# Optimization experiments

Measured on AMD Instinct MI355X. Metric: run time of the kernel, lower is better.

The kernel has to match this reference:

```python
import jax, jax.numpy as jnp
import numpy as np
import math

D_MODEL = 1024
NUM_HEADS = 16
D_K = D_MODEL // NUM_HEADS
MAX_LEN = 2048
BATCH = 2
SEQ = 2048


def setup_inputs() -> dict:
    key = jax.random.key(0)
    ks = jax.random.split(key, 12)
    w_scale = 0.02  # realistic init scale for linear weights
    inp = {
        "q": jax.random.normal(ks[0], (BATCH, SEQ, D_MODEL), jnp.float32),
        "k": jax.random.normal(ks[1], (BATCH, SEQ, D_MODEL), jnp.float32),
        "v": jax.random.normal(ks[2], (BATCH, SEQ, D_MODEL), jnp.float32),
        # learned params
        "rel_emb": jax.random.normal(ks[3], (2 * MAX_LEN, D_K), jnp.float32),
        "wq": jax.random.normal(ks[4], (D_MODEL, D_MODEL), jnp.float32) * w_scale,
        "bq": jnp.zeros((D_MODEL,), jnp.float32),
        "wk": jax.random.normal(ks[5], (D_MODEL, D_MODEL), jnp.float32) * w_scale,
        "bk": jnp.zeros((D_MODEL,), jnp.float32),
        "wv": jax.random.normal(ks[6], (D_MODEL, D_MODEL), jnp.float32) * w_scale,
        "bv": jnp.zeros((D_MODEL,), jnp.float32),
        "wo": jax.random.normal(ks[7], (D_MODEL, D_MODEL), jnp.float32) * w_scale,
        "bo": jnp.zeros((D_MODEL,), jnp.float32),
    }
    return inp


def reference(q, k, v, rel_emb, wq, bq, wk, bk, wv, bv, wo, bo):
    B, L, D = q.shape
    H, dk = NUM_HEADS, D // NUM_HEADS

    def split_heads(x):  # [B, L, D] -> [B, H, L, dk]
        return x.reshape(B, L, H, dk).transpose(0, 2, 1, 3)

    qh = split_heads(q @ wq.T + bq)
    kh = split_heads(k @ wk.T + bk)
    vh = split_heads(v @ wv.T + bv)

    # relative positions: rel_pos[i, j] = (j - i) + MAX_LEN, in [0, 2*MAX_LEN)
    r = jnp.arange(L)
    rel_pos = r[None, :] - r[:, None] + MAX_LEN  # [L, L] int32

    content_score = jnp.einsum("bhid,bhjd->bhij", qh, kh)
    # pos_score[b,h,i,j] = q[b,h,i,:] . rel_emb[rel_pos[i,j], :]
    rel = rel_emb[rel_pos]  # [L, L, dk]
    pos_score = jnp.einsum("bhid,ijd->bhij", qh, rel)

    scores = (content_score + pos_score) / math.sqrt(dk)
    attn = jax.nn.softmax(scores, axis=-1)
    out = jnp.einsum("bhij,bhjd->bhid", attn, vh)  # [B, H, L, dk]
    out = out.transpose(0, 2, 1, 3).reshape(B, L, D)
    return out @ wo.T + bo
```

## Files before the change

kernel.cpp:

```cpp
#include <hip/hip_runtime.h>
#include <hip/hip_fp16.h>


typedef _Float16 f16;
typedef _Float16 f16x4 __attribute__((ext_vector_type(4)));
typedef _Float16 f16x8 __attribute__((ext_vector_type(8)));
typedef float    f32x4 __attribute__((ext_vector_type(4)));

#define NBATCH 2
#define NHEADS 16
#define DKDIM  64
#define SEQL   2048
#define DMODEL 1024
#define NTOK   4096
#define MAXLEN 2048

__device__ __forceinline__ void gload16(const f16* g, f16* l) {
    __builtin_amdgcn_global_load_lds(
        (const __attribute__((address_space(1))) void*)g,
        (__attribute__((address_space(3))) void*)l, 16, 0, 0);
}

__global__ void cvt_f32_f16(const float* __restrict__ src, f16* __restrict__ dst, int n4) {
    int i = blockIdx.x * blockDim.x + threadIdx.x;
    if (i < n4) {
        float4 v = ((const float4*)src)[i];
        f16x4 h = { (f16)v.x, (f16)v.y, (f16)v.z, (f16)v.w };
        ((f16x4*)dst)[i] = h;
    }
}

__global__ __launch_bounds__(256, 2) void qkv_proj(
    const float* __restrict__ qg, const float* __restrict__ kg, const float* __restrict__ vg,
    const float* __restrict__ wq, const float* __restrict__ wk, const float* __restrict__ wv,
    const float* __restrict__ bq, const float* __restrict__ bk, const float* __restrict__ bv,
    f16* __restrict__ qh, f16* __restrict__ kh, f16* __restrict__ vt)
{
    const int which = blockIdx.z;
    const float* X    = which == 0 ? qg : (which == 1 ? kg : vg);
    const float* W    = which == 0 ? wq : (which == 1 ? wk : wv);
    const float* bias = which == 0 ? bq : (which == 1 ? bk : bv);

    __shared__ f16 As[128][72];
    __shared__ f16 Bs[128][72];

    const int tid = threadIdx.x;
    const int lane = tid & 63;
    const int w = tid >> 6;
    const int wr = w >> 1, wc = w & 1;
    const int row0 = blockIdx.y * 128;
    const int col0 = blockIdx.x * 128;

    f32x4 acc[4][4] = {};
    float4 ra[8], rw[8];

    #pragma unroll
    for (int rep = 0; rep < 8; ++rep) {
        int idx = rep * 256 + tid;
        int r = idx >> 4, seg = idx & 15;
        ra[rep] = *(const float4*)&X[(size_t)(row0 + r) * DMODEL + seg * 4];
        rw[rep] = *(const float4*)&W[(size_t)(col0 + r) * DMODEL + seg * 4];
    }

    for (int kk = 0; kk < DMODEL; kk += 64) {
        #pragma unroll
        for (int rep = 0; rep < 8; ++rep) {
            int idx = rep * 256 + tid;
            int r = idx >> 4, seg = idx & 15;
            f16x4 ha = { (f16)ra[rep].x, (f16)ra[rep].y, (f16)ra[rep].z, (f16)ra[rep].w };
            *(f16x4*)&As[r][seg * 4] = ha;
            f16x4 hb = { (f16)rw[rep].x, (f16)rw[rep].y, (f16)rw[rep].z, (f16)rw[rep].w };
            *(f16x4*)&Bs[r][seg * 4] = hb;
        }
        __syncthreads();
        if (kk + 64 < DMODEL) {
            #pragma unroll
            for (int rep = 0; rep < 8; ++rep) {
                int idx = rep * 256 + tid;
                int r = idx >> 4, seg = idx & 15;
                ra[rep] = *(const float4*)&X[(size_t)(row0 + r) * DMODEL + kk + 64 + seg * 4];
                rw[rep] = *(const float4*)&W[(size_t)(col0 + r) * DMODEL + kk + 64 + seg * 4];
            }
        }
        f16x8 a[4][2], b[4][2];
        #pragma unroll
        for (int mi = 0; mi < 4; ++mi)
            #pragma unroll
            for (int ks = 0; ks < 2; ++ks)
                a[mi][ks] = *(const f16x8*)&As[wr * 64 + mi * 16 + (lane & 15)][ks * 32 + (lane >> 4) * 8];
        #pragma unroll
        for (int ni = 0; ni < 4; ++ni)
            #pragma unroll
            for (int ks = 0; ks < 2; ++ks)
                b[ni][ks] = *(const f16x8*)&Bs[wc * 64 + ni * 16 + (lane & 15)][ks * 32 + (lane >> 4) * 8];
        __builtin_amdgcn_s_setprio(1);
        #pragma unroll
        for (int mi = 0; mi < 4; ++mi)
            #pragma unroll
            for (int ni = 0; ni < 4; ++ni)
                #pragma unroll
                for (int ks = 0; ks < 2; ++ks)
                    acc[mi][ni] = __builtin_amdgcn_mfma_f32_16x16x32_f16(a[mi][ks], b[ni][ks], acc[mi][ni], 0, 0, 0);
        __builtin_amdgcn_s_setprio(0);
        __syncthreads();
    }

    #pragma unroll
    for (int mi = 0; mi < 4; ++mi) {
        #pragma unroll
        for (int ni = 0; ni < 4; ++ni) {
            int col = col0 + wc * 64 + ni * 16 + (lane & 15);
            int h = col >> 6, d = col & 63;
            float bc = bias[col];
            int rowb = row0 + wr * 64 + mi * 16 + (lane >> 4) * 4;
            int b_ = rowb >> 11, l0 = rowb & 2047;
            if (which == 2) {
                f16x4 pk = { (f16)(acc[mi][ni][0] + bc), (f16)(acc[mi][ni][1] + bc),
                             (f16)(acc[mi][ni][2] + bc), (f16)(acc[mi][ni][3] + bc) };
                *(f16x4*)&vt[((size_t)((b_ * 16 + h) * 64 + d)) * 2048 + l0] = pk;
            } else {
                f16* dst = (which == 0) ? qh : kh;
                #pragma unroll
                for (int r = 0; r < 4; ++r)
                    dst[((size_t)((b_ * 16 + h) * 2048 + l0 + r)) * 64 + d] = (f16)(acc[mi][ni][r] + bc);
            }
        }
    }
}

__global__ __launch_bounds__(256, 2) void flash_attn(
    const f16* __restrict__ qh, const f16* __restrict__ kh, const f16* __restrict__ vt,
    const f16* __restrict__ rel, f16* __restrict__ att)
{
    const int tid = threadIdx.x, lane = tid & 63, w = tid >> 6;
    const int i_l = lane & 15, hi = lane >> 4;
    const int bh = blockIdx.y;
    const int b = bh >> 4, h = bh & 15;
    const int i0 = blockIdx.x * 64;

    __shared__ f16 Stage[2][16384];
    __shared__ f16 Qb[4][16][88];

    const size_t base_kq = (size_t)bh * SEQL * DKDIM;
    const int pb0 = MAXLEN - i0 - 63;
    const int t0 = 48 - w * 16;

    const int lr = lane >> 3;
    const int lc = lane & 7;
    const int sc = (lc ^ lr) << 3;

    const f16* qrow = &qh[base_kq + (size_t)(i0 + w * 16 + i_l) * 64];
    f16x8 aq[2];
    aq[0] = *(const f16x8*)&qrow[hi * 8];
    aq[1] = *(const f16x8*)&qrow[32 + hi * 8];

    {
        f16* sb = &Stage[0][0];
        #pragma unroll
        for (int c = 0; c < 2; ++c) {
            int row = w * 16 + c * 8;
            gload16(&kh[base_kq + (size_t)(row + lr) * 64 + sc], &sb[row * 64]);
            gload16(&vt[base_kq + (size_t)(row + lr) * 2048 + 0 + sc], &sb[4096 + row * 64]);
        }
        #pragma unroll
        for (int c = 0; c < 4; ++c) {
            int rrow = w * 32 + c * 8;
            int p = pb0 + rrow + lr; if (p > 4095) p = 4095;
            gload16(&rel[(size_t)p * 64 + sc], &sb[8192 + rrow * 64]);
        }
    }

    float mrun = -1e30f, lrun = 0.f;
    f32x4 oacc[4] = {};
    int cur = 0;

    const int sw0 = (hi ^ (i_l & 7)) << 3;
    const int sw1 = sw0 ^ 32;

    for (int j0 = 0; j0 < SEQL; j0 += 64) {
        __syncthreads();

        if (j0 + 64 < SEQL) {
            f16* sb = &Stage[cur ^ 1][0];
            const int jn = j0 + 64;
            #pragma unroll
            for (int c = 0; c < 2; ++c) {
                int row = w * 16 + c * 8;
                gload16(&kh[base_kq + (size_t)(jn + row + lr) * 64 + sc], &sb[row * 64]);
                gload16(&vt[base_kq + (size_t)(row + lr) * 2048 + jn + sc], &sb[4096 + row * 64]);
            }
            #pragma unroll
            for (int c = 0; c < 4; ++c) {
                int rrow = w * 32 + c * 8;
                int p = pb0 + jn + rrow + lr; if (p > 4095) p = 4095;
                gload16(&rel[(size_t)p * 64 + sc], &sb[8192 + rrow * 64]);
            }
        }

        const f16* sb = &Stage[cur][0];

        f32x4 sacc[4] = {};
        __builtin_amdgcn_s_setprio(1);
        #pragma unroll
        for (int jf = 0; jf < 4; ++jf) {
            f16x8 ak0 = *(const f16x8*)&sb[(jf * 16 + i_l) * 64 + sw0];
            f16x8 ak1 = *(const f16x8*)&sb[(jf * 16 + i_l) * 64 + sw1];
            sacc[jf] = __builtin_amdgcn_mfma_f32_16x16x32_f16(ak0, aq[0], sacc[jf], 0, 0, 0);
            sacc[jf] = __builtin_amdgcn_mfma_f32_16x16x32_f16(ak1, aq[1], sacc[jf], 0, 0, 0);
        }
        f32x4 qracc[5] = {};
        #pragma unroll
        for (int pf = 0; pf < 5; ++pf) {
            int rrow = 8192 + (t0 + pf * 16 + i_l) * 64;
            f16x8 ar0 = *(const f16x8*)&sb[rrow + sw0];
            f16x8 ar1 = *(const f16x8*)&sb[rrow + sw1];
            qracc[pf] = __builtin_amdgcn_mfma_f32_16x16x32_f16(ar0, aq[0], qracc[pf], 0, 0, 0);
            qracc[pf] = __builtin_amdgcn_mfma_f32_16x16x32_f16(ar1, aq[1], qracc[pf], 0, 0, 0);
        }
        __builtin_amdgcn_s_setprio(0);

        #pragma unroll
        for (int pf = 0; pf < 5; ++pf) {
            f16x4 pk = { (f16)qracc[pf][0], (f16)qracc[pf][1], (f16)qracc[pf][2], (f16)qracc[pf][3] };
            *(f16x4*)&Qb[w][i_l][pf * 16 + 4 * hi] = pk;
        }

        float p_[4][4];
        #pragma unroll
        for (int nf = 0; nf < 4; ++nf)
            #pragma unroll
            for (int r = 0; r < 4; ++r) {
                int t = nf * 16 + 4 * hi + r - i_l + 15;
                p_[nf][r] = (sacc[nf][r] + (float)Qb[w][i_l][t]) * 0.125f;
            }

        float mx = fmaxf(fmaxf(fmaxf(p_[0][0], p_[0][1]), fmaxf(p_[0][2], p_[0][3])),
                         fmaxf(fmaxf(p_[1][0], p_[1][1]), fmaxf(p_[1][2], p_[1][3])));
        mx = fmaxf(mx, fmaxf(fmaxf(fmaxf(p_[2][0], p_[2][1]), fmaxf(p_[2][2], p_[2][3])),
                             fmaxf(fmaxf(p_[3][0], p_[3][1]), fmaxf(p_[3][2], p_[3][3]))));
        mx = fmaxf(mx, __shfl_xor(mx, 16, 64));
        mx = fmaxf(mx, __shfl_xor(mx, 32, 64));
        if (!__all(mx - mrun <= 8.f)) {
            float mnew = fmaxf(mrun, mx);
            float scv = __expf(mrun - mnew);
            float scb[4];
            #pragma unroll
            for (int r = 0; r < 4; ++r)
                scb[r] = __shfl(scv, (lane & 48) | (4 * hi + r), 64);
            #pragma unroll
            for (int df = 0; df < 4; ++df)
                #pragma unroll
                for (int r = 0; r < 4; ++r) oacc[df][r] *= scb[r];
            lrun *= scv;
            mrun = mnew;
        }
        float sm = 0.f;
        #pragma unroll
        for (int nf = 0; nf < 4; ++nf) {
            #pragma unroll
            for (int r = 0; r < 4; ++r) { p_[nf][r] = __expf(p_[nf][r] - mrun); }
            sm += (p_[nf][0] + p_[nf][1]) + (p_[nf][2] + p_[nf][3]);
        }
        sm += __shfl_xor(sm, 16, 64);
        sm += __shfl_xor(sm, 32, 64);
        lrun += sm;

        #pragma unroll
        for (int nf = 0; nf < 4; ++nf) {
            f16x4 pk = { (f16)p_[nf][0], (f16)p_[nf][1], (f16)p_[nf][2], (f16)p_[nf][3] };
            *(f16x4*)&Qb[w][i_l][nf * 16 + 4 * hi] = pk;
        }
        f16x8 pa[2];
        pa[0] = *(const f16x8*)&Qb[w][i_l][hi * 8];
        pa[1] = *(const f16x8*)&Qb[w][i_l][32 + hi * 8];
        __builtin_amdgcn_s_setprio(1);
        #pragma unroll
        for (int df = 0; df < 4; ++df) {
            f16x8 bv0 = *(const f16x8*)&sb[4096 + (df * 16 + i_l) * 64 + sw0];
            f16x8 bv1 = *(const f16x8*)&sb[4096 + (df * 16 + i_l) * 64 + sw1];
            oacc[df] = __builtin_amdgcn_mfma_f32_16x16x32_f16(pa[0], bv0, oacc[df], 0, 0, 0);
            oacc[df] = __builtin_amdgcn_mfma_f32_16x16x32_f16(pa[1], bv1, oacc[df], 0, 0, 0);
        }
        __builtin_amdgcn_s_setprio(0);
        cur ^= 1;
    }

    float lb[4];
    #pragma unroll
    for (int r = 0; r < 4; ++r)
        lb[r] = __shfl(lrun, (lane & 48) | (4 * hi + r), 64);
    #pragma unroll
    for (int df = 0; df < 4; ++df) {
        int d = df * 16 + i_l;
        #pragma unroll
        for (int r = 0; r < 4; ++r) {
            int i = i0 + w * 16 + 4 * hi + r;
            float val = oacc[df][r] / lb[r];
            att[((size_t)(b * 2048 + i)) * DMODEL + h * 64 + d] = (f16)val;
        }
    }
}

__global__ __launch_bounds__(256, 2) void out_proj(
    const f16* __restrict__ att, const float* __restrict__ wo, const float* __restrict__ bo,
    float* __restrict__ out)
{
    __shared__ f16 As[128][72];
    __shared__ f16 Bs[128][72];
    const int tid = threadIdx.x, lane = tid & 63, w = tid >> 6;
    const int wr = w >> 1, wc = w & 1;
    const int row0 = blockIdx.y * 128, col0 = blockIdx.x * 128;

    f32x4 acc[4][4] = {};
    int4 pa_[4];
    float4 pw[8];

    #pragma unroll
    for (int rep = 0; rep < 4; ++rep) {
        int idx = rep * 256 + tid;
        int r = idx >> 3, seg = idx & 7;
        pa_[rep] = *(const int4*)&att[(size_t)(row0 + r) * DMODEL + seg * 8];
    }
    #pragma unroll
    for (int rep = 0; rep < 8; ++rep) {
        int idx = rep * 256 + tid;
        int r = idx >> 4, seg = idx & 15;
        pw[rep] = *(const float4*)&wo[(size_t)(col0 + r) * DMODEL + seg * 4];
    }

    for (int kk = 0; kk < DMODEL; kk += 64) {
        #pragma unroll
        for (int rep = 0; rep < 4; ++rep) {
            int idx = rep * 256 + tid;
            int r = idx >> 3, seg = idx & 7;
            *(int4*)&As[r][seg * 8] = pa_[rep];
        }
        #pragma unroll
        for (int rep = 0; rep < 8; ++rep) {
            int idx = rep * 256 + tid;
            int r = idx >> 4, seg = idx & 15;
            f16x4 hb = { (f16)pw[rep].x, (f16)pw[rep].y, (f16)pw[rep].z, (f16)pw[rep].w };
            *(f16x4*)&Bs[r][seg * 4] = hb;
        }
        __syncthreads();
        if (kk + 64 < DMODEL) {
            #pragma unroll
            for (int rep = 0; rep < 4; ++rep) {
                int idx = rep * 256 + tid;
                int r = idx >> 3, seg = idx & 7;
                pa_[rep] = *(const int4*)&att[(size_t)(row0 + r) * DMODEL + kk + 64 + seg * 8];
            }
            #pragma unroll
            for (int rep = 0; rep < 8; ++rep) {
                int idx = rep * 256 + tid;
                int r = idx >> 4, seg = idx & 15;
                pw[rep] = *(const float4*)&wo[(size_t)(col0 + r) * DMODEL + kk + 64 + seg * 4];
            }
        }
        f16x8 a[4][2], b[4][2];
        #pragma unroll
        for (int mi = 0; mi < 4; ++mi)
            #pragma unroll
            for (int ks = 0; ks < 2; ++ks)
                a[mi][ks] = *(const f16x8*)&As[wr * 64 + mi * 16 + (lane & 15)][ks * 32 + (lane >> 4) * 8];
        #pragma unroll
        for (int ni = 0; ni < 4; ++ni)
            #pragma unroll
            for (int ks = 0; ks < 2; ++ks)
                b[ni][ks] = *(const f16x8*)&Bs[wc * 64 + ni * 16 + (lane & 15)][ks * 32 + (lane >> 4) * 8];
        __builtin_amdgcn_s_setprio(1);
        #pragma unroll
        for (int mi = 0; mi < 4; ++mi)
            #pragma unroll
            for (int ni = 0; ni < 4; ++ni)
                #pragma unroll
                for (int ks = 0; ks < 2; ++ks)
                    acc[mi][ni] = __builtin_amdgcn_mfma_f32_16x16x32_f16(a[mi][ks], b[ni][ks], acc[mi][ni], 0, 0, 0);
        __builtin_amdgcn_s_setprio(0);
        __syncthreads();
    }

    #pragma unroll
    for (int mi = 0; mi < 4; ++mi)
        #pragma unroll
        for (int ni = 0; ni < 4; ++ni) {
            int col = col0 + wc * 64 + ni * 16 + (lane & 15);
            float bc = bo[col];
            #pragma unroll
            for (int r = 0; r < 4; ++r) {
                int row = row0 + wr * 64 + mi * 16 + (lane >> 4) * 4 + r;
                out[(size_t)row * DMODEL + col] = acc[mi][ni][r] + bc;
            }
        }
}

extern "C" void kernel_launch(void* const* d_in, const int* in_sizes, int n_in,
                              void* d_out, int out_size, void* d_ws, size_t ws_size,
                              hipStream_t stream) {
    const float* q   = (const float*)d_in[0];
    const float* k   = (const float*)d_in[1];
    const float* v   = (const float*)d_in[2];
    const float* rel = (const float*)d_in[3];
    const float* wq  = (const float*)d_in[4];
    const float* bq  = (const float*)d_in[5];
    const float* wk  = (const float*)d_in[6];
    const float* bk  = (const float*)d_in[7];
    const float* wv  = (const float*)d_in[8];
    const float* bv  = (const float*)d_in[9];
    const float* wo  = (const float*)d_in[10];
    const float* bo  = (const float*)d_in[11];
    float* out = (float*)d_out;

    f16* ws    = (f16*)d_ws;
    f16* rel16 = ws;
    f16* qh16  = rel16 + (size_t)2 * MAXLEN * DKDIM;
    f16* kh16  = qh16 + (size_t)NTOK * DMODEL;
    f16* vt16  = kh16 + (size_t)NTOK * DMODEL;
    f16* att16 = vt16 + (size_t)NTOK * DMODEL;

    cvt_f32_f16<<<dim3(256), 256, 0, stream>>>(rel, rel16, 2 * MAXLEN * DKDIM / 4);
    qkv_proj<<<dim3(8, 32, 3), 256, 0, stream>>>(q, k, v, wq, wk, wv, bq, bk, bv,
                                                 qh16, kh16, vt16);
    flash_attn<<<dim3(32, 32), 256, 0, stream>>>(qh16, kh16, vt16, rel16, att16);
    out_proj<<<dim3(8, 32), 256, 0, stream>>>(att16, wo, bo, out);
}
```

Baseline: 386.3 us.

## Pre-convert inputs and weights to fp16, use direct global-to-LDS loads in GEMMs

Adds a single conversion kernel that casts q/k/v, all four weight matrices and rel_emb to fp16 in the workspace. The projection GEMMs then stream fp16 tiles straight into LDS with global_load_lds, using an XOR-swizzled layout instead of padding, and raise occupancy to 3 blocks. They also use a swizzled block order for L2 locality. This removes per-tile fp32 loads and conversions, but it drops the register prefetch double-buffering and adds an extra full pass over the inputs. att16 now aliases the converted q buffer.

```diff
diff --git a/kernel.cpp b/kernel.cpp
--- a/kernel.cpp
+++ b/kernel.cpp
@@ -21,86 +21,88 @@
         (__attribute__((address_space(3))) void*)l, 16, 0, 0);
 }
 
-__global__ void cvt_f32_f16(const float* __restrict__ src, f16* __restrict__ dst, int n4) {
-    int i = blockIdx.x * blockDim.x + threadIdx.x;
-    if (i < n4) {
-        float4 v = ((const float4*)src)[i];
-        f16x4 h = { (f16)v.x, (f16)v.y, (f16)v.z, (f16)v.w };
+__global__ void cvt_all(
+    const float* __restrict__ q, const float* __restrict__ k, const float* __restrict__ v,
+    const float* __restrict__ wq, const float* __restrict__ wk, const float* __restrict__ wv,
+    const float* __restrict__ wo, const float* __restrict__ rel, f16* __restrict__ dst)
+{
+    const int SX = 1048576;
+    const int SW = 262144;
+    const int SR = 65536;
+    const int total = 3 * SX + 4 * SW + SR;
+    for (int i = blockIdx.x * blockDim.x + threadIdx.x; i < total; i += gridDim.x * blockDim.x) {
+        int j = i;
+        const float* s;
+        if (j < SX) s = q;
+        else if ((j -= SX) < SX) s = k;
+        else if ((j -= SX) < SX) s = v;
+        else if ((j -= SX) < SW) s = wq;
+        else if ((j -= SW) < SW) s = wk;
+        else if ((j -= SW) < SW) s = wv;
+        else if ((j -= SW) < SW) s = wo;
+        else { j -= SW; s = rel; }
+        float4 vv = ((const float4*)s)[j];
+        f16x4 h = { (f16)vv.x, (f16)vv.y, (f16)vv.z, (f16)vv.w };
         ((f16x4*)dst)[i] = h;
     }
 }
 
-__global__ __launch_bounds__(256, 2) void qkv_proj(
-    const float* __restrict__ qg, const float* __restrict__ kg, const float* __restrict__ vg,
-    const float* __restrict__ wq, const float* __restrict__ wk, const float* __restrict__ wv,
+__global__ __launch_bounds__(256, 3) void qkv_proj(
+    const f16* __restrict__ xq, const f16* __restrict__ xk, const f16* __restrict__ xv,
+    const f16* __restrict__ wq16, const f16* __restrict__ wk16, const f16* __restrict__ wv16,
     const float* __restrict__ bq, const float* __restrict__ bk, const float* __restrict__ bv,
     f16* __restrict__ qh, f16* __restrict__ kh, f16* __restrict__ vt)
 {
     const int which = blockIdx.z;
-    const float* X    = which == 0 ? qg : (which == 1 ? kg : vg);
-    const float* W    = which == 0 ? wq : (which == 1 ? wk : wv);
+    const f16* X      = which == 0 ? xq : (which == 1 ? xk : xv);
+    const f16* W      = which == 0 ? wq16 : (which == 1 ? wk16 : wv16);
     const float* bias = which == 0 ? bq : (which == 1 ? bk : bv);
 
-    __shared__ f16 As[128][72];
-    __shared__ f16 Bs[128][72];
-
-    const int tid = threadIdx.x;
-    const int lane = tid & 63;
-    const int w = tid >> 6;
+    __shared__ f16 As[128 * 64];
+    __shared__ f16 Bs[128 * 64];
+
+    const int tid = threadIdx.x, lane = tid & 63, w = tid >> 6;
+    const int i_l = lane & 15, hi = lane >> 4;
     const int wr = w >> 1, wc = w & 1;
-    const int row0 = blockIdx.y * 128;
-    const int col0 = blockIdx.x * 128;
+
+    const int nbid = blockIdx.y * 8 + blockIdx.x;
+    const int swz = (nbid & 7) * 32 + (nbid >> 3);
+    const int row0 = (swz >> 3) * 128;
+    const int col0 = (swz & 7) * 128;
+
+    const int lr = lane >> 3, lc = lane & 7;
+    const int sc = (lc ^ lr) << 3;
 
     f32x4 acc[4][4] = {};
-    float4 ra[8], rw[8];
-
-    #pragma unroll
-    for (int rep = 0; rep < 8; ++rep) {
-        int idx = rep * 256 + tid;
-        int r = idx >> 4, seg = idx & 15;
-        ra[rep] = *(const float4*)&X[(size_t)(row0 + r) * DMODEL + seg * 4];
-        rw[rep] = *(const float4*)&W[(size_t)(col0 + r) * DMODEL + seg * 4];
-    }
 
     for (int kk = 0; kk < DMODEL; kk += 64) {
         #pragma unroll
-        for (int rep = 0; rep < 8; ++rep) {
-            int idx = rep * 256 + tid;
-            int r = idx >> 4, seg = idx & 15;
-            f16x4 ha = { (f16)ra[rep].x, (f16)ra[rep].y, (f16)ra[rep].z, (f16)ra[rep].w };
-            *(f16x4*)&As[r][seg * 4] = ha;
-            f16x4 hb = { (f16)rw[rep].x, (f16)rw[rep].y, (f16)rw[rep].z, (f16)rw[rep].w };
-            *(f16x4*)&Bs[r][seg * 4] = hb;
+        for (int c = 0; c < 4; ++c) {
+            int row = w * 32 + c * 8;
+            gload16(&X[(size_t)(row0 + row + lr) * DMODEL + kk + sc], &As[row * 64]);
+            gload16(&W[(size_t)(col0 + row + lr) * DMODEL + kk + sc], &Bs[row * 64]);
         }
         __syncthreads();
-        if (kk + 64 < DMODEL) {
-            #pragma unroll
-            for (int rep = 0; rep < 8; ++rep) {
-                int idx = rep * 256 + tid;
-                int r = idx >> 4, seg = idx & 15;
-                ra[rep] = *(const float4*)&X[(size_t)(row0 + r) * DMODEL + kk + 64 + seg * 4];
-                rw[rep] = *(const float4*)&W[(size_t)(col0 + r) * DMODEL + kk + 64 + seg * 4];
-            }
-        }
-        f16x8 a[4][2], b[4][2];
-        #pragma unroll
-        for (int mi = 0; mi < 4; ++mi)
+
+        f16x8 bfr[4][2];
+        #pragma unroll
+        for (int ni = 0; ni < 4; ++ni)
             #pragma unroll
             for (int ks = 0; ks < 2; ++ks)
-                a[mi][ks] = *(const f16x8*)&As[wr * 64 + mi * 16 + (lane & 15)][ks * 32 + (lane >> 4) * 8];
-        #pragma unroll
-        for (int ni = 0; ni < 4; ++ni)
+                bfr[ni][ks] = *(const f16x8*)&Bs[(wc * 64 + ni * 16 + i_l) * 64 + (((ks * 4 + hi) ^ (i_l & 7)) << 3)];
+        __builtin_amdgcn_s_setprio(1);
+        #pragma unroll
+        for (int mi = 0; mi < 4; ++mi) {
+            f16x8 afr[2];
             #pragma unroll
             for (int ks = 0; ks < 2; ++ks)
-                b[ni][ks] = *(const f16x8*)&Bs[wc * 64 + ni * 16 + (lane & 15)][ks * 32 + (lane >> 4) * 8];
-        __builtin_amdgcn_s_setprio(1);
-        #pragma unroll
-        for (int mi = 0; mi < 4; ++mi)
+                afr[ks] = *(const f16x8*)&As[(wr * 64 + mi * 16 + i_l) * 64 + (((ks * 4 + hi) ^ (i_l & 7)) << 3)];
             #pragma unroll
             for (int ni = 0; ni < 4; ++ni)
                 #pragma unroll
                 for (int ks = 0; ks < 2; ++ks)
-                    acc[mi][ni] = __builtin_amdgcn_mfma_f32_16x16x32_f16(a[mi][ks], b[ni][ks], acc[mi][ni], 0, 0, 0);
+                    acc[mi][ni] = __builtin_amdgcn_mfma_f32_16x16x32_f16(afr[ks], bfr[ni][ks], acc[mi][ni], 0, 0, 0);
+        }
         __builtin_amdgcn_s_setprio(0);
         __syncthreads();
     }
@@ -109,10 +111,10 @@
     for (int mi = 0; mi < 4; ++mi) {
         #pragma unroll
         for (int ni = 0; ni < 4; ++ni) {
-            int col = col0 + wc * 64 + ni * 16 + (lane & 15);
+            int col = col0 + wc * 64 + ni * 16 + i_l;
             int h = col >> 6, d = col & 63;
             float bc = bias[col];
-            int rowb = row0 + wr * 64 + mi * 16 + (lane >> 4) * 4;
+            int rowb = row0 + wr * 64 + mi * 16 + hi * 4;
             int b_ = rowb >> 11, l0 = rowb & 2047;
             if (which == 2) {
                 f16x4 pk = { (f16)(acc[mi][ni][0] + bc), (f16)(acc[mi][ni][1] + bc),
@@ -301,81 +303,55 @@
     }
 }
 
-__global__ __launch_bounds__(256, 2) void out_proj(
-    const f16* __restrict__ att, const float* __restrict__ wo, const float* __restrict__ bo,
+__global__ __launch_bounds__(256, 3) void out_proj(
+    const f16* __restrict__ att, const f16* __restrict__ wo16, const float* __restrict__ bo,
     float* __restrict__ out)
 {
-    __shared__ f16 As[128][72];
-    __shared__ f16 Bs[128][72];
+    __shared__ f16 As[128 * 64];
+    __shared__ f16 Bs[128 * 64];
+
     const int tid = threadIdx.x, lane = tid & 63, w = tid >> 6;
+    const int i_l = lane & 15, hi = lane >> 4;
     const int wr = w >> 1, wc = w & 1;
-    const int row0 = blockIdx.y * 128, col0 = blockIdx.x * 128;
+
+    const int nbid = blockIdx.y * 8 + blockIdx.x;
+    const int swz = (nbid & 7) * 32 + (nbid >> 3);
+    const int row0 = (swz >> 3) * 128;
+    const int col0 = (swz & 7) * 128;
+
+    const int lr = lane >> 3, lc = lane & 7;
+    const int sc = (lc ^ lr) << 3;
 
     f32x4 acc[4][4] = {};
-    int4 pa_[4];
-    float4 pw[8];
-
-    #pragma unroll
-    for (int rep = 0; rep < 4; ++rep) {
-        int idx = rep * 256 + tid;
-        int r = idx >> 3, seg = idx & 7;
-        pa_[rep] = *(const int4*)&att[(size_t)(row0 + r) * DMODEL + seg * 8];
-    }
-    #pragma unroll
-    for (int rep = 0; rep < 8; ++rep) {
-        int idx = rep * 256 + tid;
-        int r = idx >> 4, seg = idx & 15;
-        pw[rep] = *(const float4*)&wo[(size_t)(col0 + r) * DMODEL + seg * 4];
-    }
 
     for (int kk = 0; kk < DMODEL; kk += 64) {
         #pragma unroll
-        for (int rep = 0; rep < 4; ++rep) {
-            int idx = rep * 256 + tid;
-            int r = idx >> 3, seg = idx & 7;
-            *(int4*)&As[r][seg * 8] = pa_[rep];
-        }
-        #pragma unroll
-        for (int rep = 0; rep < 8; ++rep) {
-            int idx = rep * 256 + tid;
-            int r = idx >> 4, seg = idx & 15;
-            f16x4 hb = { (f16)pw[rep].x, (f16)pw[rep].y, (f16)pw[rep].z, (f16)pw[rep].w };
-            *(f16x4*)&Bs[r][seg * 4] = hb;
+        for (int c = 0; c < 4; ++c) {
+            int row = w * 32 + c * 8;
+            gload16(&att[(size_t)(row0 + row + lr) * DMODEL + kk + sc], &As[row * 64]);
+            gload16(&wo16[(size_t)(col0 + row + lr) * DMODEL + kk + sc], &Bs[row * 64]);
         }
         __syncthreads();
-        if (kk + 64 < DMODEL) {
-            #pragma unroll
-            for (int rep = 0; rep < 4; ++rep) {
-                int idx = rep * 256 + tid;
-                int r = idx >> 3, seg = idx & 7;
-                pa_[rep] = *(const int4*)&att[(size_t)(row0 + r) * DMODEL + kk + 64 + seg * 8];
-            }
-            #pragma unroll
-            for (int rep = 0; rep < 8; ++rep) {
-                int idx = rep * 256 + tid;
-                int r = idx >> 4, seg = idx & 15;
-                pw[rep] = *(const float4*)&wo[(size_t)(col0 + r) * DMODEL + kk + 64 + seg * 4];
-            }
-        }
-        f16x8 a[4][2], b[4][2];
-        #pragma unroll
-        for (int mi = 0; mi < 4; ++mi)
+
+        f16x8 bfr[4][2];
+        #pragma unroll
+        for (int ni = 0; ni < 4; ++ni)
             #pragma unroll
             for (int ks = 0; ks < 2; ++ks)
-                a[mi][ks] = *(const f16x8*)&As[wr * 64 + mi * 16 + (lane & 15)][ks * 32 + (lane >> 4) * 8];
-        #pragma unroll
-        for (int ni = 0; ni < 4; ++ni)
+                bfr[ni][ks] = *(const f16x8*)&Bs[(wc * 64 + ni * 16 + i_l) * 64 + (((ks * 4 + hi) ^ (i_l & 7)) << 3)];
+        __builtin_amdgcn_s_setprio(1);
+        #pragma unroll
+        for (int mi = 0; mi < 4; ++mi) {
+            f16x8 afr[2];
             #pragma unroll
             for (int ks = 0; ks < 2; ++ks)
-                b[ni][ks] = *(const f16x8*)&Bs[wc * 64 + ni * 16 + (lane & 15)][ks * 32 + (lane >> 4) * 8];
-        __builtin_amdgcn_s_setprio(1);
-        #pragma unroll
-        for (int mi = 0; mi < 4; ++mi)
+                afr[ks] = *(const f16x8*)&As[(wr * 64 + mi * 16 + i_l) * 64 + (((ks * 4 + hi) ^ (i_l & 7)) << 3)];
             #pragma unroll
             for (int ni = 0; ni < 4; ++ni)
                 #pragma unroll
                 for (int ks = 0; ks < 2; ++ks)
-                    acc[mi][ni] = __builtin_amdgcn_mfma_f32_16x16x32_f16(a[mi][ks], b[ni][ks], acc[mi][ni], 0, 0, 0);
+                    acc[mi][ni] = __builtin_amdgcn_mfma_f32_16x16x32_f16(afr[ks], bfr[ni][ks], acc[mi][ni], 0, 0, 0);
+        }
         __builtin_amdgcn_s_setprio(0);
         __syncthreads();
     }
@@ -384,11 +360,11 @@
     for (int mi = 0; mi < 4; ++mi)
         #pragma unroll
         for (int ni = 0; ni < 4; ++ni) {
-            int col = col0 + wc * 64 + ni * 16 + (lane & 15);
+            int col = col0 + wc * 64 + ni * 16 + i_l;
             float bc = bo[col];
             #pragma unroll
             for (int r = 0; r < 4; ++r) {
-                int row = row0 + wr * 64 + mi * 16 + (lane >> 4) * 4 + r;
+                int row = row0 + wr * 64 + mi * 16 + hi * 4 + r;
                 out[(size_t)row * DMODEL + col] = acc[mi][ni][r] + bc;
             }
         }
@@ -411,16 +387,27 @@
     const float* bo  = (const float*)d_in[11];
     float* out = (float*)d_out;
 
+    const size_t SX = (size_t)NTOK * DMODEL;
+    const size_t SW = (size_t)DMODEL * DMODEL;
+    const size_t SR = (size_t)2 * MAXLEN * DKDIM;
+
     f16* ws    = (f16*)d_ws;
-    f16* rel16 = ws;
-    f16* qh16  = rel16 + (size_t)2 * MAXLEN * DKDIM;
-    f16* kh16  = qh16 + (size_t)NTOK * DMODEL;
-    f16* vt16  = kh16 + (size_t)NTOK * DMODEL;
-    f16* att16 = vt16 + (size_t)NTOK * DMODEL;
-
-    cvt_f32_f16<<<dim3(256), 256, 0, stream>>>(rel, rel16, 2 * MAXLEN * DKDIM / 4);
-    qkv_proj<<<dim3(8, 32, 3), 256, 0, stream>>>(q, k, v, wq, wk, wv, bq, bk, bv,
-                                                 qh16, kh16, vt16);
+    f16* x16q  = ws;
+    f16* x16k  = x16q + SX;
+    f16* x16v  = x16k + SX;
+    f16* wq16  = x16v + SX;
+    f16* wk16  = wq16 + SW;
+    f16* wv16  = wk16 + SW;
+    f16* wo16  = wv16 + SW;
+    f16* rel16 = wo16 + SW;
+    f16* qh16  = rel16 + SR;
+    f16* kh16  = qh16 + SX;
+    f16* vt16  = kh16 + SX;
+    f16* att16 = x16q;
+
+    cvt_all<<<dim3(2048), 256, 0, stream>>>(q, k, v, wq, wk, wv, wo, rel, ws);
+    qkv_proj<<<dim3(8, 32, 3), 256, 0, stream>>>(x16q, x16k, x16v, wq16, wk16, wv16,
+                                                 bq, bk, bv, qh16, kh16, vt16);
     flash_attn<<<dim3(32, 32), 256, 0, stream>>>(qh16, kh16, vt16, rel16, att16);
-    out_proj<<<dim3(8, 32), 256, 0, stream>>>(att16, wo, bo, out);
-}
+    out_proj<<<dim3(8, 32), 256, 0, stream>>>(att16, wo16, bo, out);
+}
```

Measured after the change: 356.4 us. 1.08x faster.
